# Kernel tuning notes

Hardware: AMD Instinct MI355X
Metric: run time of the kernel (lower is better)

The kernel has to match this reference:

```python
import jax, jax.numpy as jnp
import numpy as np

V, E, H, C, T = 100000, 300, 512, 40, 4096  # vocab, embed, hidden, num_classes, seq_len


def setup_inputs() -> dict:
    key = jax.random.key(0)
    ks = jax.random.split(key, 19)
    s = lambda k, shape: jax.random.normal(k, shape, jnp.float32) * 0.05
    inp = {"x": jax.random.randint(ks[0], (T,), 0, V, dtype=jnp.int32)}
    inp["emb"] = s(ks[1], (V, E))  # frozen embedding table
    # PyTorch LSTM params, gate order (i, f, g, o); layer0 in=E, layer1 in=2H
    inp["Wih0f"] = s(ks[2], (4 * H, E)); inp["Whh0f"] = s(ks[3], (4 * H, H)); inp["b0f"] = s(ks[4], (4 * H,))
    inp["Wih0b"] = s(ks[5], (4 * H, E)); inp["Whh0b"] = s(ks[6], (4 * H, H)); inp["b0b"] = s(ks[7], (4 * H,))
    inp["Wih1f"] = s(ks[8], (4 * H, 2 * H)); inp["Whh1f"] = s(ks[9], (4 * H, H)); inp["b1f"] = s(ks[10], (4 * H,))
    inp["Wih1b"] = s(ks[11], (4 * H, 2 * H)); inp["Whh1b"] = s(ks[12], (4 * H, H)); inp["b1b"] = s(ks[13], (4 * H,))
    inp["Wc"] = s(ks[14], (C, 2 * H)); inp["bc"] = s(ks[15], (C,))
    inp["trans"] = s(ks[16], (C, C))  # CRF transitions prev->next
    inp["start"] = s(ks[17], (C,)); inp["end"] = s(ks[18], (C,))
    return inp


def _lstm_dir(x, Wih, Whh, b, reverse):
    # x: (T, D) unbatched; returns hidden states (T, H)
    Hd = Whh.shape[1]
    def step(carry, xt):
        h, c = carry
        g = xt @ Wih.T + h @ Whh.T + b  # (4H,)
        i, f, gg, o = jnp.split(g, 4)
        i = jax.nn.sigmoid(i); f = jax.nn.sigmoid(f)
        gg = jnp.tanh(gg); o = jax.nn.sigmoid(o)
        c = f * c + i * gg
        h = o * jnp.tanh(c)
        return (h, c), h
    xs = x[::-1] if reverse else x
    init = (jnp.zeros((Hd,), x.dtype), jnp.zeros((Hd,), x.dtype))
    _, hs = jax.lax.scan(step, init, xs)
    return hs[::-1] if reverse else hs


def _viterbi(emissions, trans, start, end):
    # emissions: (T, C); returns best path (T,) int32
    def fwd(score, em):
        m = score[:, None] + trans  # (C_prev, C_next)
        bp = jnp.argmax(m, axis=0).astype(jnp.int32)
        return jnp.max(m, axis=0) + em, bp
    score0 = start + emissions[0]
    final, bps = jax.lax.scan(fwd, score0, emissions[1:])  # bps: (T-1, C)
    last = jnp.argmax(final + end).astype(jnp.int32)
    def back(tag, bp):
        prev = bp[tag]
        return prev, prev
    _, path = jax.lax.scan(back, last, bps, reverse=True)  # tags 0..T-2 in order
    return jnp.concatenate([path, last[None]])


def reference(x, emb, Wih0f, Whh0f, b0f, Wih0b, Whh0b, b0b, Wih1f, Whh1f, b1f, Wih1b, Whh1b, b1b, Wc, bc, trans, start, end):
    e = emb[x]  # (T, E); dropout is identity at eval
    h0 = jnp.concatenate([_lstm_dir(e, Wih0f, Whh0f, b0f, False),
                          _lstm_dir(e, Wih0b, Whh0b, b0b, True)], axis=-1)  # (T, 2H)
    h1 = jnp.concatenate([_lstm_dir(h0, Wih1f, Whh1f, b1f, False),
                          _lstm_dir(h0, Wih1b, Whh1b, b1b, True)], axis=-1)  # (T, 2H)
    o = h1 @ Wc.T + bc  # (T, C)
    tag_scores = jax.nn.log_softmax(o, axis=1)
    tags = _viterbi(tag_scores, trans, start, end)
    return tag_scores, tags
```

## Files before the change

### kernel.cpp

```cpp
#include <hip/hip_runtime.h>


typedef unsigned int u32;
typedef unsigned long long u64;

#define TT 4096
#define HH 512
#define CC 40
#define NG 2048

__device__ __forceinline__ float sigm(float x) { return 1.0f / (1.0f + __expf(-x)); }
__device__ __forceinline__ float tanh_(float x) { return 1.0f - 2.0f / (__expf(2.0f * x) + 1.0f); }

__device__ __forceinline__ void st_agent_u32(u32* p, u32 v) {
    __hip_atomic_store(p, v, __ATOMIC_RELAXED, __HIP_MEMORY_SCOPE_AGENT);
}
__device__ __forceinline__ u64 ld_agent_u64(const u64* p) {
    return __hip_atomic_load((u64*)p, __ATOMIC_RELAXED, __HIP_MEMORY_SCOPE_AGENT);
}

__global__ __launch_bounds__(256, 2) void gemm_f32_k(const float* __restrict__ A0,
                                                     const float* __restrict__ A1,
                                                     const int* __restrict__ xidx,
                                                     const float* __restrict__ W,
                                                     const float* __restrict__ bias,
                                                     float* __restrict__ C,
                                                     int M, int N, int K, int Ksplit) {
    __shared__ float sA[32][66];
    __shared__ float sW[32][66];
    int tid = threadIdx.x;
    int bn = blockIdx.x, bm = blockIdx.y;
    int tx = tid & 15, ty = tid >> 4;
    int srow = tid >> 2, skk = (tid & 3) * 8;

    int am = bm * 64 + srow;
    const float* arow0;
    const float* arow1 = nullptr;
    if (xidx) {
        arow0 = A0 + (size_t)xidx[am] * K;
    } else {
        arow0 = A0 + (size_t)am * Ksplit;
        arow1 = A1 + (size_t)am * Ksplit;
    }
    const float* wrow = W + (size_t)(bn * 64 + srow) * K;

    float acc[4][4] = {};

    for (int kc = 0; kc < K; kc += 32) {
        float av[8], wv[8];
        if (kc + 32 <= K) {
#pragma unroll
            for (int j = 0; j < 8; j++) {
                int k = kc + skk + j;
                av[j] = (xidx || k < Ksplit) ? arow0[k] : arow1[k - Ksplit];
                wv[j] = wrow[k];
            }
        } else {
#pragma unroll
            for (int j = 0; j < 8; j++) {
                int k = kc + skk + j;
                bool ok = k < K;
                av[j] = (ok ? ((xidx || k < Ksplit) ? arow0[k] : arow1[k - Ksplit]) : 0.f);
                wv[j] = ok ? wrow[k] : 0.f;
            }
        }
        __syncthreads();
#pragma unroll
        for (int j = 0; j < 8; j++) {
            sA[skk + j][srow] = av[j];
            sW[skk + j][srow] = wv[j];
        }
        __syncthreads();
#pragma unroll
        for (int k = 0; k < 32; k++) {
            float4 a4 = *(const float4*)&sA[k][ty * 4];
            float4 w4 = *(const float4*)&sW[k][tx * 4];
            acc[0][0] += a4.x * w4.x; acc[0][1] += a4.x * w4.y; acc[0][2] += a4.x * w4.z; acc[0][3] += a4.x * w4.w;
            acc[1][0] += a4.y * w4.x; acc[1][1] += a4.y * w4.y; acc[1][2] += a4.y * w4.z; acc[1][3] += a4.y * w4.w;
            acc[2][0] += a4.z * w4.x; acc[2][1] += a4.z * w4.y; acc[2][2] += a4.z * w4.z; acc[2][3] += a4.z * w4.w;
            acc[3][0] += a4.w * w4.x; acc[3][1] += a4.w * w4.y; acc[3][2] += a4.w * w4.z; acc[3][3] += a4.w * w4.w;
        }
    }

    int gm = bm * 64 + ty * 4;
    int gn = bn * 64 + tx * 4;
    float4 b4 = *(const float4*)&bias[gn];
#pragma unroll
    for (int mi = 0; mi < 4; mi++) {
        float4 o;
        o.x = acc[mi][0] + b4.x; o.y = acc[mi][1] + b4.y;
        o.z = acc[mi][2] + b4.z; o.w = acc[mi][3] + b4.w;
        *(float4*)&C[(size_t)(gm + mi) * N + gn] = o;
    }
}

__global__ __attribute__((amdgpu_flat_work_group_size(512, 512), amdgpu_waves_per_eu(2, 2)))
void lstm_phase_k(const float* __restrict__ WxF,
                  const float* __restrict__ WxB,
                  const float* __restrict__ WhhF,
                  const float* __restrict__ WhhB,
                  float* __restrict__ histF,
                  float* __restrict__ histB,
                  int phase) {
    const int wg = blockIdx.x & 31;
    const int dir = blockIdx.x >> 5;
    const int tid = threadIdx.x;
    const float* Wx = dir ? WxB : WxF;
    const float* Whh = dir ? WhhB : WhhF;
    float* hist = dir ? histB : histF;
    const u32 ENC = phase ? 0x7F800000u : 0u;

    const int r = tid >> 3, seg = tid & 7;
    const int grow = (r >> 4) * 512 + wg * 16 + (r & 15);

    float w[64];
    {
        const float* wr = Whh + (size_t)grow * HH + seg * 64;
#pragma unroll
        for (int i = 0; i < 16; i++) {
            float4 v = *(const float4*)(wr + i * 4);
            w[i * 4 + 0] = v.x; w[i * 4 + 1] = v.y; w[i * 4 + 2] = v.z; w[i * 4 + 3] = v.w;
        }
    }

    const int j = (tid < 124) ? (tid + (tid >= wg * 4 ? 4 : 0)) : 0;

    __shared__ float lds_h[8 * 68];
    __shared__ float lds_g[64];
    float c_state = 0.f;
    int capped = 0;

    for (int s = 0; s < TT; ++s) {
        const int t = dir ? (TT - 1 - s) : s;
        float wxv = 0.f;
        if (seg == 0) wxv = Wx[(size_t)t * NG + grow];

        if (s > 0) {
            const int tprev = dir ? (t + 1) : (t - 1);
            if (tid < 124) {
                const u64* p = (const u64*)(hist + (size_t)tprev * HH) + j * 2;
                u64 v0, v1;
                if (!capped) {
                    int it = 0;
                    for (;;) {
                        v0 = ld_agent_u64(p);
                        v1 = ld_agent_u64(p + 1);
                        u32 a = (u32)v0, b = (u32)(v0 >> 32), c = (u32)v1, d = (u32)(v1 >> 32);
                        bool ok = phase
                            ? (((a & 0x7F800000u) >= 0x40000000u) && ((b & 0x7F800000u) >= 0x40000000u) &&
                               ((c & 0x7F800000u) >= 0x40000000u) && ((d & 0x7F800000u) >= 0x40000000u))
                            : ((a != 0xAAAAAAAAu) && (b != 0xAAAAAAAAu) &&
                               (c != 0xAAAAAAAAu) && (d != 0xAAAAAAAAu));
                        if (ok) break;
                        if (++it > (1 << 19)) { capped = 1; break; }
                    }
                } else {
                    v0 = ld_agent_u64(p);
                    v1 = ld_agent_u64(p + 1);
                }
                float4 hv;
                hv.x = __uint_as_float((u32)v0 ^ ENC);
                hv.y = __uint_as_float((u32)(v0 >> 32) ^ ENC);
                hv.z = __uint_as_float((u32)v1 ^ ENC);
                hv.w = __uint_as_float((u32)(v1 >> 32) ^ ENC);
                *(float4*)&lds_h[(j >> 4) * 68 + ((j * 4) & 63)] = hv;
            }
            __syncthreads();
            float a0 = 0.f, a1 = 0.f, a2 = 0.f, a3 = 0.f;
            const float4* hv4 = (const float4*)&lds_h[seg * 68];
#pragma unroll
            for (int i = 0; i < 16; i++) {
                float4 hv = hv4[i];
                a0 += w[i * 4 + 0] * hv.x;
                a1 += w[i * 4 + 1] * hv.y;
                a2 += w[i * 4 + 2] * hv.z;
                a3 += w[i * 4 + 3] * hv.w;
            }
            float acc = (a0 + a1) + (a2 + a3);
            acc += __shfl_xor(acc, 1);
            acc += __shfl_xor(acc, 2);
            acc += __shfl_xor(acc, 4);
            if (seg == 0) lds_g[r] = acc + wxv;
        } else {
            if (seg == 0) lds_g[r] = wxv;
        }
        __syncthreads();

        if (tid < 16) {
            float gi = lds_g[tid], gf = lds_g[16 + tid], gg = lds_g[32 + tid], go = lds_g[48 + tid];
            float iv = sigm(gi), fv = sigm(gf), gv = tanh_(gg), ov = sigm(go);
            c_state = fv * c_state + iv * gv;
            float h = ov * tanh_(c_state);
            int hidx = wg * 16 + tid;
            lds_h[(hidx >> 6) * 68 + (hidx & 63)] = h;
            st_agent_u32((u32*)&hist[(size_t)t * HH + hidx], __float_as_uint(h) ^ ENC);
        }
    }
}

__global__ __launch_bounds__(64, 4) void classifier_k(const float* __restrict__ histF,
                                                      const float* __restrict__ histB,
                                                      const float* __restrict__ Wc,
                                                      const float* __restrict__ bc,
                                                      float* __restrict__ outsc) {
    int t = blockIdx.x, lane = threadIdx.x;
    __shared__ float hrow[1024];
    const uint4* hf4 = (const uint4*)(histF + (size_t)t * HH);
    const uint4* hb4 = (const uint4*)(histB + (size_t)t * HH);
#pragma unroll
    for (int jj = 0; jj < 4; jj++) {
        int idx4 = jj * 64 + lane;
        uint4 u = (idx4 < 128) ? hf4[idx4] : hb4[idx4 - 128];
        u.x ^= 0x7F800000u; u.y ^= 0x7F800000u; u.z ^= 0x7F800000u; u.w ^= 0x7F800000u;
        float4 v;
        v.x = __uint_as_float(u.x); v.y = __uint_as_float(u.y);
        v.z = __uint_as_float(u.z); v.w = __uint_as_float(u.w);
        *(float4*)&hrow[idx4 * 4] = v;
    }
    __syncthreads();
    float o = 0.f;
    if (lane < CC) {
        o = bc[lane];
        const float4* wr = (const float4*)(Wc + (size_t)lane * 1024);
#pragma unroll 4
        for (int kk = 0; kk < 256; ++kk) {
            float4 w4 = wr[kk];
            float4 h4 = *(const float4*)&hrow[kk * 4];
            o += w4.x * h4.x + w4.y * h4.y + w4.z * h4.z + w4.w * h4.w;
        }
    }
    float m = (lane < CC) ? o : -1e30f;
#pragma unroll
    for (int d = 1; d < 64; d <<= 1) m = fmaxf(m, __shfl_xor(m, d));
    float ex = (lane < CC) ? __expf(o - m) : 0.f;
#pragma unroll
    for (int d = 1; d < 64; d <<= 1) ex += __shfl_xor(ex, d);
    float lse = m + __logf(ex);
    if (lane < CC) outsc[(size_t)t * CC + lane] = o - lse;
}

__global__ __launch_bounds__(64) void viterbi_k(const float* __restrict__ em,
                                               const float* __restrict__ trans,
                                               const float* __restrict__ startv,
                                               const float* __restrict__ endv,
                                               unsigned char* __restrict__ bp,
                                               float* __restrict__ outtags) {
    int lane = threadIdx.x;
    float tcol[CC];
#pragma unroll
    for (int p = 0; p < CC; p++) tcol[p] = 0.f;
    if (lane < CC) {
#pragma unroll
        for (int p = 0; p < CC; p++) tcol[p] = trans[p * CC + lane];
    }
    float s = (lane < CC) ? (startv[lane] + em[lane]) : 0.f;

    for (int t = 1; t < TT; ++t) {
        float emv = (lane < CC) ? em[(size_t)t * CC + lane] : 0.f;
        float b0 = -1e30f, b1 = -1e30f;
        int i0 = 0, i1 = 20;
#pragma unroll
        for (int p = 0; p < 20; p++) {
            float c0 = __shfl(s, p) + tcol[p];
            float c1 = __shfl(s, p + 20) + tcol[p + 20];
            if (c0 > b0) { b0 = c0; i0 = p; }
            if (c1 > b1) { b1 = c1; i1 = p + 20; }
        }
        float best = b0; int bi = i0;
        if (b1 > b0) { best = b1; bi = i1; }
        s = best + emv;
        if (lane < CC) bp[(size_t)t * CC + lane] = (unsigned char)bi;
    }
    float fv = (lane < CC) ? (s + endv[lane]) : -1e30f;
    int fi = (lane < CC) ? lane : 63;
#pragma unroll
    for (int d = 1; d < 64; d <<= 1) {
        float ov = __shfl_xor(fv, d);
        int oi = __shfl_xor(fi, d);
        if (ov > fv || (ov == fv && oi < fi)) { fv = ov; fi = oi; }
    }
    __threadfence();
    if (lane == 0) {
        int cur = fi;
        outtags[TT - 1] = (float)cur;
        for (int t = TT - 2; t >= 0; --t) {
            cur = bp[(size_t)(t + 1) * CC + cur];
            outtags[t] = (float)cur;
        }
    }
}

extern "C" void kernel_launch(void* const* d_in, const int* in_sizes, int n_in,
                              void* d_out, int out_size, void* d_ws, size_t ws_size,
                              hipStream_t stream) {
    const int*   x     = (const int*)d_in[0];
    const float* emb   = (const float*)d_in[1];
    const float* Wih0f = (const float*)d_in[2];
    const float* Whh0f = (const float*)d_in[3];
    const float* b0f   = (const float*)d_in[4];
    const float* Wih0b = (const float*)d_in[5];
    const float* Whh0b = (const float*)d_in[6];
    const float* b0b   = (const float*)d_in[7];
    const float* Wih1f = (const float*)d_in[8];
    const float* Whh1f = (const float*)d_in[9];
    const float* b1f   = (const float*)d_in[10];
    const float* Wih1b = (const float*)d_in[11];
    const float* Whh1b = (const float*)d_in[12];
    const float* b1b   = (const float*)d_in[13];
    const float* Wc    = (const float*)d_in[14];
    const float* bc    = (const float*)d_in[15];
    const float* trans = (const float*)d_in[16];
    const float* startv= (const float*)d_in[17];
    const float* endv  = (const float*)d_in[18];

    char* ws = (char*)d_ws;
    unsigned char* bp = (unsigned char*)(ws + 1024);
    float* WxF  = (float*)(ws + 262144);
    float* WxB  = (float*)(ws + 33816576);
    float* histF= (float*)(ws + 67371008);
    float* histB= (float*)(ws + 75759616);

    if (ws_size < (size_t)84148224) return;

    float* out_sc   = (float*)d_out;
    float* out_tags = out_sc + (size_t)TT * CC;

    gemm_f32_k<<<dim3(32, 64), 256, 0, stream>>>(emb, nullptr, x, Wih0f, b0f, WxF, TT, NG, 300, 300);
    gemm_f32_k<<<dim3(32, 64), 256, 0, stream>>>(emb, nullptr, x, Wih0b, b0b, WxB, TT, NG, 300, 300);
    lstm_phase_k<<<64, 512, 0, stream>>>(WxF, WxB, Whh0f, Whh0b, histF, histB, 0);
    gemm_f32_k<<<dim3(32, 64), 256, 0, stream>>>(histF, histB, nullptr, Wih1f, b1f, WxF, TT, NG, 1024, 512);
    gemm_f32_k<<<dim3(32, 64), 256, 0, stream>>>(histF, histB, nullptr, Wih1b, b1b, WxB, TT, NG, 1024, 512);
    lstm_phase_k<<<64, 512, 0, stream>>>(WxF, WxB, Whh1f, Whh1b, histF, histB, 1);
    classifier_k<<<TT, 64, 0, stream>>>(histF, histB, Wc, bc, out_sc);
    viterbi_k<<<1, 64, 0, stream>>>(out_sc, trans, startv, endv, bp, out_tags);
}
```

Baseline: 19.45 ms.

## Widen LSTM hidden-state polling loads and enlarge GEMM tiles to 128x128

The recurrent LSTM kernel now polls the previous hidden state with fewer threads. Each thread issues two 16-byte loads through inline assembly with sc0/sc1 cache-coherence bits, replacing two 64-bit agent-scope atomic loads, which should cut per-step handoff latency on the serial critical path. The poll iteration cap is also halved. Separately, the input-projection GEMM moves from 64x64 to 128x128 output tiles with an 8-deep K chunk and vectorized float4 global loads, raising arithmetic intensity at the cost of more registers per thread and fewer blocks in the grid.

```diff
diff --git a/kernel.cpp b/kernel.cpp
--- a/kernel.cpp
+++ b/kernel.cpp
@@ -3,6 +3,7 @@
 
 typedef unsigned int u32;
 typedef unsigned long long u64;
+typedef u32 u32x4 __attribute__((ext_vector_type(4)));
 
 #define TT 4096
 #define HH 512
@@ -15,8 +16,15 @@
 __device__ __forceinline__ void st_agent_u32(u32* p, u32 v) {
     __hip_atomic_store(p, v, __ATOMIC_RELAXED, __HIP_MEMORY_SCOPE_AGENT);
 }
-__device__ __forceinline__ u64 ld_agent_u64(const u64* p) {
-    return __hip_atomic_load((u64*)p, __ATOMIC_RELAXED, __HIP_MEMORY_SCOPE_AGENT);
+
+__device__ __forceinline__ void ld_mall_b256(const float* p, u32x4& r0, u32x4& r1) {
+    asm volatile(
+        "global_load_dwordx4 %0, %2, off sc0 sc1\n\t"
+        "global_load_dwordx4 %1, %2, off offset:16 sc0 sc1\n\t"
+        "s_waitcnt vmcnt(0)"
+        : "=&v"(r0), "=&v"(r1)
+        : "v"(p)
+        : "memory");
 }
 
 __global__ __launch_bounds__(256, 2) void gemm_f32_k(const float* __restrict__ A0,
@@ -26,14 +34,14 @@
                                                      const float* __restrict__ bias,
                                                      float* __restrict__ C,
                                                      int M, int N, int K, int Ksplit) {
-    __shared__ float sA[32][66];
-    __shared__ float sW[32][66];
+    __shared__ float sA[8][132];
+    __shared__ float sW[8][132];
     int tid = threadIdx.x;
     int bn = blockIdx.x, bm = blockIdx.y;
     int tx = tid & 15, ty = tid >> 4;
-    int srow = tid >> 2, skk = (tid & 3) * 8;
-
-    int am = bm * 64 + srow;
+    int srow = tid >> 1, skh = (tid & 1) * 4;
+
+    int am = bm * 128 + srow;
     const float* arow0;
     const float* arow1 = nullptr;
     if (xidx) {
@@ -42,55 +50,70 @@
         arow0 = A0 + (size_t)am * Ksplit;
         arow1 = A1 + (size_t)am * Ksplit;
     }
-    const float* wrow = W + (size_t)(bn * 64 + srow) * K;
-
-    float acc[4][4] = {};
-
-    for (int kc = 0; kc < K; kc += 32) {
-        float av[8], wv[8];
-        if (kc + 32 <= K) {
-#pragma unroll
-            for (int j = 0; j < 8; j++) {
-                int k = kc + skk + j;
-                av[j] = (xidx || k < Ksplit) ? arow0[k] : arow1[k - Ksplit];
-                wv[j] = wrow[k];
+    const float* wrow = W + (size_t)(bn * 128 + srow) * K;
+
+    float acc[2][2][4][4] = {};
+
+    for (int kc = 0; kc < K; kc += 8) {
+        float4 av, wv;
+        int k0 = kc + skh;
+        if (kc + 8 <= K) {
+            if (xidx || k0 + 4 <= Ksplit) av = *(const float4*)(arow0 + k0);
+            else                          av = *(const float4*)(arow1 + (k0 - Ksplit));
+            wv = *(const float4*)(wrow + k0);
+        } else {
+            float a_[4], w_[4];
+#pragma unroll
+            for (int j = 0; j < 4; j++) {
+                int k = k0 + j;
+                bool ok = k < K;
+                a_[j] = ok ? ((xidx || k < Ksplit) ? arow0[k] : arow1[k - Ksplit]) : 0.f;
+                w_[j] = ok ? wrow[k] : 0.f;
             }
-        } else {
-#pragma unroll
-            for (int j = 0; j < 8; j++) {
-                int k = kc + skk + j;
-                bool ok = k < K;
-                av[j] = (ok ? ((xidx || k < Ksplit) ? arow0[k] : arow1[k - Ksplit]) : 0.f);
-                wv[j] = ok ? wrow[k] : 0.f;
+            av = make_float4(a_[0], a_[1], a_[2], a_[3]);
+            wv = make_float4(w_[0], w_[1], w_[2], w_[3]);
+        }
+        __syncthreads();
+        sA[skh + 0][srow] = av.x; sA[skh + 1][srow] = av.y;
+        sA[skh + 2][srow] = av.z; sA[skh + 3][srow] = av.w;
+        sW[skh + 0][srow] = wv.x; sW[skh + 1][srow] = wv.y;
+        sW[skh + 2][srow] = wv.z; sW[skh + 3][srow] = wv.w;
+        __syncthreads();
+#pragma unroll
+        for (int k = 0; k < 8; k++) {
+            float4 a0 = *(const float4*)&sA[k][ty * 4];
+            float4 a1 = *(const float4*)&sA[k][64 + ty * 4];
+            float4 w0 = *(const float4*)&sW[k][tx * 4];
+            float4 w1 = *(const float4*)&sW[k][64 + tx * 4];
+            float am_[2][4] = {{a0.x, a0.y, a0.z, a0.w}, {a1.x, a1.y, a1.z, a1.w}};
+            float wn_[2][4] = {{w0.x, w0.y, w0.z, w0.w}, {w1.x, w1.y, w1.z, w1.w}};
+#pragma unroll
+            for (int p = 0; p < 2; p++)
+#pragma unroll
+                for (int q = 0; q < 2; q++)
+#pragma unroll
+                    for (int mi = 0; mi < 4; mi++)
+#pragma unroll
+                        for (int ni = 0; ni < 4; ni++)
+                            acc[p][q][mi][ni] += am_[p][mi] * wn_[q][ni];
+        }
+    }
+
+#pragma unroll
+    for (int q = 0; q < 2; q++) {
+        int gn = bn * 128 + q * 64 + tx * 4;
+        float4 b4 = *(const float4*)&bias[gn];
+#pragma unroll
+        for (int p = 0; p < 2; p++) {
+            int gm = bm * 128 + p * 64 + ty * 4;
+#pragma unroll
+            for (int mi = 0; mi < 4; mi++) {
+                float4 o;
+                o.x = acc[p][q][mi][0] + b4.x; o.y = acc[p][q][mi][1] + b4.y;
+                o.z = acc[p][q][mi][2] + b4.z; o.w = acc[p][q][mi][3] + b4.w;
+                *(float4*)&C[(size_t)(gm + mi) * N + gn] = o;
             }
         }
-        __syncthreads();
-#pragma unroll
-        for (int j = 0; j < 8; j++) {
-            sA[skk + j][srow] = av[j];
-            sW[skk + j][srow] = wv[j];
-        }
-        __syncthreads();
-#pragma unroll
-        for (int k = 0; k < 32; k++) {
-            float4 a4 = *(const float4*)&sA[k][ty * 4];
-            float4 w4 = *(const float4*)&sW[k][tx * 4];
-            acc[0][0] += a4.x * w4.x; acc[0][1] += a4.x * w4.y; acc[0][2] += a4.x * w4.z; acc[0][3] += a4.x * w4.w;
-            acc[1][0] += a4.y * w4.x; acc[1][1] += a4.y * w4.y; acc[1][2] += a4.y * w4.z; acc[1][3] += a4.y * w4.w;
-            acc[2][0] += a4.z * w4.x; acc[2][1] += a4.z * w4.y; acc[2][2] += a4.z * w4.z; acc[2][3] += a4.z * w4.w;
-            acc[3][0] += a4.w * w4.x; acc[3][1] += a4.w * w4.y; acc[3][2] += a4.w * w4.z; acc[3][3] += a4.w * w4.w;
-        }
-    }
-
-    int gm = bm * 64 + ty * 4;
-    int gn = bn * 64 + tx * 4;
-    float4 b4 = *(const float4*)&bias[gn];
-#pragma unroll
-    for (int mi = 0; mi < 4; mi++) {
-        float4 o;
-        o.x = acc[mi][0] + b4.x; o.y = acc[mi][1] + b4.y;
-        o.z = acc[mi][2] + b4.z; o.w = acc[mi][3] + b4.w;
-        *(float4*)&C[(size_t)(gm + mi) * N + gn] = o;
     }
 }
 
@@ -123,7 +146,7 @@
         }
     }
 
-    const int j = (tid < 124) ? (tid + (tid >= wg * 4 ? 4 : 0)) : 0;
+    const int j = (tid < 62) ? (tid + (tid >= wg * 2 ? 2 : 0)) : 0;
 
     __shared__ float lds_h[8 * 68];
     __shared__ float lds_g[64];
@@ -137,33 +160,43 @@
 
         if (s > 0) {
             const int tprev = dir ? (t + 1) : (t - 1);
-            if (tid < 124) {
-                const u64* p = (const u64*)(hist + (size_t)tprev * HH) + j * 2;
-                u64 v0, v1;
+            if (tid < 62) {
+                const float* p = hist + (size_t)tprev * HH + j * 8;
+                u32x4 v0, v1;
                 if (!capped) {
                     int it = 0;
                     for (;;) {
-                        v0 = ld_agent_u64(p);
-                        v1 = ld_agent_u64(p + 1);
-                        u32 a = (u32)v0, b = (u32)(v0 >> 32), c = (u32)v1, d = (u32)(v1 >> 32);
-                        bool ok = phase
-                            ? (((a & 0x7F800000u) >= 0x40000000u) && ((b & 0x7F800000u) >= 0x40000000u) &&
-                               ((c & 0x7F800000u) >= 0x40000000u) && ((d & 0x7F800000u) >= 0x40000000u))
-                            : ((a != 0xAAAAAAAAu) && (b != 0xAAAAAAAAu) &&
-                               (c != 0xAAAAAAAAu) && (d != 0xAAAAAAAAu));
+                        ld_mall_b256(p, v0, v1);
+                        bool ok;
+                        if (phase) {
+                            ok = ((v0.x & 0x7F800000u) >= 0x40000000u) &&
+                                 ((v0.y & 0x7F800000u) >= 0x40000000u) &&
+                                 ((v0.z & 0x7F800000u) >= 0x40000000u) &&
+                                 ((v0.w & 0x7F800000u) >= 0x40000000u) &&
+                                 ((v1.x & 0x7F800000u) >= 0x40000000u) &&
+                                 ((v1.y & 0x7F800000u) >= 0x40000000u) &&
+                                 ((v1.z & 0x7F800000u) >= 0x40000000u) &&
+                                 ((v1.w & 0x7F800000u) >= 0x40000000u);
+                        } else {
+                            ok = (v0.x != 0xAAAAAAAAu) && (v0.y != 0xAAAAAAAAu) &&
+                                 (v0.z != 0xAAAAAAAAu) && (v0.w != 0xAAAAAAAAu) &&
+                                 (v1.x != 0xAAAAAAAAu) && (v1.y != 0xAAAAAAAAu) &&
+                                 (v1.z != 0xAAAAAAAAu) && (v1.w != 0xAAAAAAAAu);
+                        }
                         if (ok) break;
-                        if (++it > (1 << 19)) { capped = 1; break; }
+                        if (++it > (1 << 18)) { capped = 1; break; }
                     }
                 } else {
-                    v0 = ld_agent_u64(p);
-                    v1 = ld_agent_u64(p + 1);
+                    ld_mall_b256(p, v0, v1);
                 }
-                float4 hv;
-                hv.x = __uint_as_float((u32)v0 ^ ENC);
-                hv.y = __uint_as_float((u32)(v0 >> 32) ^ ENC);
-                hv.z = __uint_as_float((u32)v1 ^ ENC);
-                hv.w = __uint_as_float((u32)(v1 >> 32) ^ ENC);
-                *(float4*)&lds_h[(j >> 4) * 68 + ((j * 4) & 63)] = hv;
+                float* dst = &lds_h[(j >> 3) * 68 + ((j & 7) * 8)];
+                float4 f0, f1;
+                f0.x = __uint_as_float(v0.x ^ ENC); f0.y = __uint_as_float(v0.y ^ ENC);
+                f0.z = __uint_as_float(v0.z ^ ENC); f0.w = __uint_as_float(v0.w ^ ENC);
+                f1.x = __uint_as_float(v1.x ^ ENC); f1.y = __uint_as_float(v1.y ^ ENC);
+                f1.z = __uint_as_float(v1.z ^ ENC); f1.w = __uint_as_float(v1.w ^ ENC);
+                *(float4*)dst = f0;
+                *(float4*)(dst + 4) = f1;
             }
             __syncthreads();
             float a0 = 0.f, a1 = 0.f, a2 = 0.f, a3 = 0.f;
@@ -325,11 +358,11 @@
     float* out_sc   = (float*)d_out;
     float* out_tags = out_sc + (size_t)TT * CC;
 
-    gemm_f32_k<<<dim3(32, 64), 256, 0, stream>>>(emb, nullptr, x, Wih0f, b0f, WxF, TT, NG, 300, 300);
-    gemm_f32_k<<<dim3(32, 64), 256, 0, stream>>>(emb, nullptr, x, Wih0b, b0b, WxB, TT, NG, 300, 300);
+    gemm_f32_k<<<dim3(16, 32), 256, 0, stream>>>(emb, nullptr, x, Wih0f, b0f, WxF, TT, NG, 300, 300);
+    gemm_f32_k<<<dim3(16, 32), 256, 0, stream>>>(emb, nullptr, x, Wih0b, b0b, WxB, TT, NG, 300, 300);
     lstm_phase_k<<<64, 512, 0, stream>>>(WxF, WxB, Whh0f, Whh0b, histF, histB, 0);
-    gemm_f32_k<<<dim3(32, 64), 256, 0, stream>>>(histF, histB, nullptr, Wih1f, b1f, WxF, TT, NG, 1024, 512);
-    gemm_f32_k<<<dim3(32, 64), 256, 0, stream>>>(histF, histB, nullptr, Wih1b, b1b, WxB, TT, NG, 1024, 512);
+    gemm_f32_k<<<dim3(16, 32), 256, 0, stream>>>(histF, histB, nullptr, Wih1f, b1f, WxF, TT, NG, 1024, 512);
+    gemm_f32_k<<<dim3(16, 32), 256, 0, stream>>>(histF, histB, nullptr, Wih1b, b1b, WxB, TT, NG, 1024, 512);
     lstm_phase_k<<<64, 512, 0, stream>>>(WxF, WxB, Whh1f, Whh1b, histF, histB, 1);
     classifier_k<<<TT, 64, 0, stream>>>(histF, histB, Wc, bc, out_sc);
     viterbi_k<<<1, 64, 0, stream>>>(out_sc, trans, startv, endv, bp, out_tags);
```

Result: faster. 17.66 ms (-9.2%).
